# Performance work log

Measured on AMD Instinct MI355X. Metric: run time of the kernel, lower is better.

## Reference

```python
import jax, jax.numpy as jnp
import numpy as np

N = 100000      # nodes
E = 1600000     # edges
NG = 512        # graphs in batch
FIN = 7         # in_features
HID = 128       # hidden_channels
OUT = 2         # outfeatures


def setup_inputs() -> dict:
    key = jax.random.key(0)
    ks = jax.random.split(key, 16)
    x = jax.random.normal(ks[0], (N, FIN), jnp.float32)
    edge_index = jax.random.randint(ks[1], (2, E), 0, N, dtype=jnp.int64)
    batch = jnp.sort(jax.random.randint(ks[2], (N,), 0, NG, dtype=jnp.int64))

    def lin_w(k, fan_in, fan_out):
        # glorot-ish init, scale irrelevant for correctness baseline
        return jax.random.normal(k, (fan_in, fan_out), jnp.float32) / np.sqrt(fan_in).astype(np.float32)

    W1 = lin_w(ks[3], FIN, HID); b1 = jnp.zeros((HID,), jnp.float32)
    W2 = lin_w(ks[4], HID, HID); b2 = jnp.zeros((HID,), jnp.float32)
    W3 = lin_w(ks[5], HID, HID); b3 = jnp.zeros((HID,), jnp.float32)
    W4 = lin_w(ks[6], HID, HID); b4 = jnp.zeros((HID,), jnp.float32)
    Wlin = lin_w(ks[7], HID, OUT); blin = jnp.zeros((OUT,), jnp.float32)
    return dict(x=x, edge_index=edge_index, batch=batch,
                W1=W1, b1=b1, W2=W2, b2=b2, W3=W3, b3=b3, W4=W4, b4=b4,
                Wlin=Wlin, blin=blin)


def gcn_conv(h, W, b, src, dst, n):
    # PyG GCNConv: h' = D^{-1/2} (A + I) D^{-1/2} (h W) + b
    # src/dst already include self-loops
    h = h @ W
    deg = jax.ops.segment_sum(jnp.ones(src.shape[0], h.dtype), dst, num_segments=n)
    dinv = jnp.where(deg > 0, jax.lax.rsqrt(deg), jnp.zeros_like(deg))
    norm = dinv[src] * dinv[dst]                       # [E+N]
    agg = jax.ops.segment_sum(norm[:, None] * h[src], dst, num_segments=n)
    return agg + b


def reference(x, edge_index, batch, W1, b1, W2, b2, W3, b3, W4, b4, Wlin, blin):
    loop = jnp.arange(N, dtype=edge_index.dtype)
    src = jnp.concatenate([edge_index[0], loop])       # add self-loops
    dst = jnp.concatenate([edge_index[1], loop])

    h = gcn_conv(x, W1, b1, src, dst, N)
    for W, b in ((W2, b2), (W3, b3), (W4, b4)):
        h = jax.nn.relu(h)
        h = gcn_conv(h, W, b, src, dst, N)

    # global mean pool per graph
    sums = jax.ops.segment_sum(h, batch, num_segments=NG)
    cnt = jax.ops.segment_sum(jnp.ones((N,), h.dtype), batch, num_segments=NG)
    pooled = sums / jnp.maximum(cnt, 1.0)[:, None]     # [NG, HID]

    # dropout is identity in eval mode
    return pooled @ Wlin + blin                        # [NG, OUT]
```

## Files before the change

### kernel.cpp

```cpp
#include <hip/hip_runtime.h>
#include <hip/hip_bf16.h>

#define N_NODES 100000
#define E_EDGES 1600000
#define NG 512
#define FIN 7
#define HID 128
#define NBUCK 782
#define NBLK_SC 256
#define CHUNK 6250
#define TLEN (NBUCK * NBLK_SC)
#define NCH 196
#define MMX_GRID 782
#define AGGW_GRID 25000

typedef __attribute__((ext_vector_type(8))) short bf16x8;
typedef __attribute__((ext_vector_type(4))) float f32x4;

__device__ __forceinline__ float bf_lo(unsigned int u) { return __uint_as_float(u << 16); }
__device__ __forceinline__ float bf_hi(unsigned int u) { return __uint_as_float(u & 0xffff0000u); }
__device__ __forceinline__ unsigned int f2bf_rne(float f) {
    unsigned int x = __float_as_uint(f);
    return (x + 0x7fffu + ((x >> 16) & 1u)) >> 16;
}
__device__ __forceinline__ unsigned int pack_bf2(float lo, float hi) {
    return f2bf_rne(lo) | (f2bf_rne(hi) << 16);
}


__global__ __launch_bounds__(256) void k_hist2(const int* __restrict__ eidx,
                                               int* __restrict__ table,
                                               const float* __restrict__ W4,
                                               const float* __restrict__ b4,
                                               const float* __restrict__ Wlin,
                                               const float* __restrict__ blin,
                                               float* __restrict__ Wc,
                                               float* __restrict__ bc,
                                               float* __restrict__ pooled,
                                               const float* __restrict__ W2,
                                               const float* __restrict__ W3,
                                               unsigned short* __restrict__ WT2,
                                               unsigned short* __restrict__ WT3) {
    __shared__ int h[NBUCK];
    int blk = blockIdx.x, t = threadIdx.x;
    if (blk >= NBLK_SC) {
        int r = blk - NBLK_SC;
        if (r < 64) {
            float4 z = {0.f, 0.f, 0.f, 0.f};
            *(float4*)&pooled[(r * 256 + t) * 4] = z;
        } else if (r == 64) {
            int k = t >> 1, o = t & 1;
            float acc = 0.f;
            for (int j = 0; j < HID; ++j) acc += W4[k * HID + j] * Wlin[j * 2 + o];
            Wc[k * 2 + o] = acc;
            if (k == 0) {
                float b = blin[o];
                for (int j = 0; j < HID; ++j) b += b4[j] * Wlin[j * 2 + o];
                bc[o] = b;
            }
        } else if (r < 129) {
            int idx = (r - 65) * 256 + t;
            int k = idx >> 7, n = idx & 127;
            WT2[n * 128 + k] = (unsigned short)f2bf_rne(W2[idx]);
        } else {
            int idx = (r - 129) * 256 + t;
            int k = idx >> 7, n = idx & 127;
            WT3[n * 128 + k] = (unsigned short)f2bf_rne(W3[idx]);
        }
        return;
    }
    for (int i = t; i < NBUCK; i += 256) h[i] = 0;
    __syncthreads();
    int e0 = blk * CHUNK, e1 = e0 + CHUNK;
    for (int e = e0 + t; e < e1; e += 256)
        atomicAdd(&h[eidx[E_EDGES + e] >> 7], 1);
    __syncthreads();
    for (int i = t; i < NBUCK; i += 256)
        table[i * NBLK_SC + blk] = h[i];
}

__global__ void k_blocksum(const int* __restrict__ table, int* __restrict__ partial) {
    __shared__ int s[256];
    int b = blockIdx.x, t = threadIdx.x;
    int base = b * 1024;
    int sum = 0;
    for (int i = t; i < 1024; i += 256) {
        int idx = base + i;
        sum += (idx < TLEN) ? table[idx] : 0;
    }
    s[t] = sum; __syncthreads();
    for (int st = 128; st > 0; st >>= 1) {
        if (t < st) s[t] += s[t + st];
        __syncthreads();
    }
    if (t == 0) partial[b] = s[0];
}

__global__ void k_scan_blk(int* __restrict__ partial, int* __restrict__ bucketBase,
                           int* __restrict__ rowptr) {
    __shared__ int s[256];
    int t = threadIdx.x;
    int v = (t < NCH) ? partial[t] : 0;
    s[t] = v; __syncthreads();
    for (int st = 1; st < 256; st <<= 1) {
        int a = (t >= st) ? s[t - st] : 0;
        __syncthreads();
        s[t] += a;
        __syncthreads();
    }
    if (t < NCH) partial[t] = s[t] - v;
    if (t == 0) { bucketBase[NBUCK] = E_EDGES; rowptr[N_NODES] = E_EDGES; }
}

__global__ void k_scan_final(int* __restrict__ table, const int* __restrict__ partial,
                             int* __restrict__ bucketBase) {
    __shared__ int s[1024];
    int b = blockIdx.x, t = threadIdx.x;
    int idx = b * 1024 + t;
    int v = (idx < TLEN) ? table[idx] : 0;
    s[t] = v; __syncthreads();
    for (int st = 1; st < 1024; st <<= 1) {
        int add = (t >= st) ? s[t - st] : 0;
        __syncthreads();
        s[t] += add;
        __syncthreads();
    }
    if (idx < TLEN) {
        int ex = partial[b] + s[t] - v;
        table[idx] = ex;
        if ((idx & (NBLK_SC - 1)) == 0) bucketBase[idx / NBLK_SC] = ex;
    }
}

__global__ __launch_bounds__(256) void k_scatter2(const int* __restrict__ eidx,
                                                  const int* __restrict__ table,
                                                  unsigned int* __restrict__ ebuf) {
    __shared__ int loff[NBUCK];
    int blk = blockIdx.x, t = threadIdx.x;
    for (int i = t; i < NBUCK; i += 256) loff[i] = table[i * NBLK_SC + blk];
    __syncthreads();
    int e0 = blk * CHUNK, e1 = e0 + CHUNK;
    for (int e = e0 + t; e < e1; e += 256) {
        int s = eidx[e];
        int d = eidx[E_EDGES + e];
        int p = atomicAdd(&loff[d >> 7], 1);
        ebuf[p] = ((unsigned int)(d & 127) << 17) | (unsigned int)s;
    }
}

__global__ __launch_bounds__(256) void k_bucket(const unsigned int* __restrict__ ebuf,
                                                const int* __restrict__ bucketBase,
                                                int* __restrict__ rowptr,
                                                float* __restrict__ dinv,
                                                int* __restrict__ col) {
    __shared__ int scnt[128], soff[128], scur[128];
    int b = blockIdx.x, t = threadIdx.x;
    int bbase = bucketBase[b], bend = bucketBase[b + 1];
    if (t < 128) { scnt[t] = 0; scur[t] = 0; }
    __syncthreads();
    for (int e = bbase + t; e < bend; e += 256) {
        unsigned int rec = ebuf[e];
        atomicAdd(&scnt[rec >> 17], 1);
    }
    __syncthreads();
    if (t < 128) soff[t] = scnt[t];
    __syncthreads();
    for (int st = 1; st < 128; st <<= 1) {
        int a = (t < 128 && t >= st) ? soff[t - st] : 0;
        __syncthreads();
        if (t < 128) soff[t] += a;
        __syncthreads();
    }
    if (t < 128) {
        int ex = soff[t] - scnt[t];
        int node = b * 128 + t;
        if (node < N_NODES) {
            rowptr[node] = bbase + ex;
            dinv[node] = rsqrtf((float)(scnt[t] + 1));
        }
        soff[t] = ex;
    }
    __syncthreads();
    for (int e = bbase + t; e < bend; e += 256) {
        unsigned int rec = ebuf[e];
        int dl = rec >> 17;
        int s = rec & 0x1FFFF;
        int p = bbase + soff[dl] + atomicAdd(&scur[dl], 1);
        col[p] = s;
    }
}


__global__ __launch_bounds__(256) void k_l1(const float* __restrict__ x,
                                            const float* __restrict__ W1,
                                            const float* __restrict__ b1,
                                            const int* __restrict__ rowptr,
                                            const int* __restrict__ col,
                                            const float* __restrict__ dinv,
                                            unsigned int* __restrict__ g1) {
    __shared__ float axs[32][8];
    __shared__ float w1s[FIN * HID];
    __shared__ float b1s[HID];
    int t = threadIdx.x;
    for (int i = t; i < FIN * HID; i += 256) w1s[i] = W1[i];
    if (t < HID) b1s[t] = b1[t];

    int lane = t & 63, wave = t >> 6;
    int sub = lane >> 3, f = lane & 7;
    int node = blockIdx.x * 32 + wave * 8 + sub;
    bool valid = node < N_NODES;
    float di = valid ? dinv[node] : 0.f;
    float a = (valid && f < 7) ? di * x[node * FIN + f] : 0.f;
    int e0 = valid ? rowptr[node] : 0;
    int e1 = valid ? rowptr[node + 1] : 0;
    for (int base = e0; base < e1; base += 8) {
        int mm = e1 - base; if (mm > 8) mm = 8;
        int sc = (f < mm) ? col[base + f] : 0;
        for (int j = 0; j < mm; ++j) {
            int s = __shfl(sc, sub * 8 + j);
            float v = (f < 7) ? x[s * FIN + f] : dinv[s];
            float ds = __shfl(v, sub * 8 + 7);
            if (f < 7) a += ds * v;
        }
    }
    axs[wave * 8 + sub][f] = (f < 7) ? di * a : 0.f;
    __syncthreads();

    int nl = t >> 3, fb = t & 7;
    int gnode = blockIdx.x * 32 + nl;
    if (gnode < N_NODES) {
        float av[FIN];
        #pragma unroll
        for (int k = 0; k < FIN; ++k) av[k] = axs[nl][k];
        float dsc = dinv[gnode];
        unsigned int outp[8];
        #pragma unroll
        for (int p = 0; p < 8; ++p) {
            int fo = fb * 16 + p * 2;
            float acc0 = b1s[fo], acc1 = b1s[fo + 1];
            #pragma unroll
            for (int k = 0; k < FIN; ++k) {
                acc0 += av[k] * w1s[k * HID + fo];
                acc1 += av[k] * w1s[k * HID + fo + 1];
            }
            outp[p] = pack_bf2(dsc * fmaxf(acc0, 0.f), dsc * fmaxf(acc1, 0.f));
        }
        *(uint4*)&g1[(size_t)gnode * 64 + fb * 8] = *(uint4*)&outp[0];
        *(uint4*)&g1[(size_t)gnode * 64 + fb * 8 + 4] = *(uint4*)&outp[4];
    }
}


__global__ __launch_bounds__(256) void k_aggW(const unsigned int* __restrict__ gIn,
                                              unsigned int* __restrict__ gOut,
                                              const int* __restrict__ rowptr,
                                              const int* __restrict__ colv,
                                              const float* __restrict__ dinv) {
    int wid = (blockIdx.x * blockDim.x + threadIdx.x) >> 6;
    int lane = threadIdx.x & 63;
    if (wid >= N_NODES) return;
    int i = wid;
    float di = dinv[i];
    int e0 = rowptr[i], e1 = rowptr[i + 1];
    int cv = colv[e0 + lane];
    unsigned int v = gIn[(size_t)i * 64 + lane];
    float ax = bf_lo(v), ay = bf_hi(v);

    for (int base = e0; base < e1; base += 64) {
        int m = e1 - base; if (m > 64) m = 64;
        int cvn = cv;
        if (base + 64 < e1) cvn = colv[base + 64 + lane];
        int j = 0;
        for (; j + 7 < m; j += 8) {
            int s0 = __shfl(cv, j),     s1 = __shfl(cv, j + 1);
            int s2 = __shfl(cv, j + 2), s3 = __shfl(cv, j + 3);
            int s4 = __shfl(cv, j + 4), s5 = __shfl(cv, j + 5);
            int s6 = __shfl(cv, j + 6), s7 = __shfl(cv, j + 7);
            unsigned int u0 = gIn[(size_t)s0 * 64 + lane];
            unsigned int u1 = gIn[(size_t)s1 * 64 + lane];
            unsigned int u2 = gIn[(size_t)s2 * 64 + lane];
            unsigned int u3 = gIn[(size_t)s3 * 64 + lane];
            unsigned int u4 = gIn[(size_t)s4 * 64 + lane];
            unsigned int u5 = gIn[(size_t)s5 * 64 + lane];
            unsigned int u6 = gIn[(size_t)s6 * 64 + lane];
            unsigned int u7 = gIn[(size_t)s7 * 64 + lane];
            ax += bf_lo(u0); ay += bf_hi(u0);
            ax += bf_lo(u1); ay += bf_hi(u1);
            ax += bf_lo(u2); ay += bf_hi(u2);
            ax += bf_lo(u3); ay += bf_hi(u3);
            ax += bf_lo(u4); ay += bf_hi(u4);
            ax += bf_lo(u5); ay += bf_hi(u5);
            ax += bf_lo(u6); ay += bf_hi(u6);
            ax += bf_lo(u7); ay += bf_hi(u7);
        }
        for (; j + 3 < m; j += 4) {
            int s0 = __shfl(cv, j),     s1 = __shfl(cv, j + 1);
            int s2 = __shfl(cv, j + 2), s3 = __shfl(cv, j + 3);
            unsigned int u0 = gIn[(size_t)s0 * 64 + lane];
            unsigned int u1 = gIn[(size_t)s1 * 64 + lane];
            unsigned int u2 = gIn[(size_t)s2 * 64 + lane];
            unsigned int u3 = gIn[(size_t)s3 * 64 + lane];
            ax += bf_lo(u0); ay += bf_hi(u0);
            ax += bf_lo(u1); ay += bf_hi(u1);
            ax += bf_lo(u2); ay += bf_hi(u2);
            ax += bf_lo(u3); ay += bf_hi(u3);
        }
        for (; j < m; ++j) {
            int s0 = __shfl(cv, j);
            unsigned int u0 = gIn[(size_t)s0 * 64 + lane];
            ax += bf_lo(u0); ay += bf_hi(u0);
        }
        cv = cvn;
    }
    gOut[(size_t)i * 64 + lane] = pack_bf2(di * ax, di * ay);
}


__global__ __launch_bounds__(256) void k_mmx(const unsigned int* __restrict__ gIn,
                                             const unsigned short* __restrict__ WTg,
                                             const float* __restrict__ bias,
                                             const float* __restrict__ dinv,
                                             unsigned int* __restrict__ outg) {
    __shared__ unsigned short sbuf[128 * 136];
    int t = threadIdx.x;
    for (int i = t * 8; i < 128 * 128; i += 256 * 8) {
        int n = i >> 7, k = i & 127;
        uint4 val = *(const uint4*)(WTg + i);
        *(uint4*)(sbuf + n * 136 + k) = val;
    }

    int lane = t & 63, wave = t >> 6;
    int m = lane & 15, quad = lane >> 4;
    int nodeBase = blockIdx.x * 128 + wave * 32;
    const short* gs = (const short*)gIn;

    float bi[8];
    #pragma unroll
    for (int nt = 0; nt < 8; ++nt) bi[nt] = bias[nt * 16 + m];

    f32x4 acc[2][8];
    #pragma unroll
    for (int gi = 0; gi < 2; ++gi)
        #pragma unroll
        for (int nt = 0; nt < 8; ++nt)
            acc[gi][nt] = (f32x4){0.f, 0.f, 0.f, 0.f};

    __syncthreads();

    #pragma unroll
    for (int kc = 0; kc < 4; ++kc) {
        bf16x8 ah[2];
        #pragma unroll
        for (int gi = 0; gi < 2; ++gi) {
            int node = nodeBase + gi * 16 + m;
            bf16x8 h = {0, 0, 0, 0, 0, 0, 0, 0};
            if (node < N_NODES)
                h = *(const bf16x8*)(gs + (size_t)node * 128 + kc * 32 + quad * 8);
            ah[gi] = h;
        }
        #pragma unroll
        for (int nt = 0; nt < 8; ++nt) {
            bf16x8 b = *(const bf16x8*)(sbuf + (nt * 16 + m) * 136 + kc * 32 + quad * 8);
            #pragma unroll
            for (int gi = 0; gi < 2; ++gi)
                acc[gi][nt] = __builtin_amdgcn_mfma_f32_16x16x32_bf16(ah[gi], b, acc[gi][nt], 0, 0, 0);
        }
    }

    __syncthreads();
    #pragma unroll
    for (int gi = 0; gi < 2; ++gi)
        #pragma unroll
        for (int r = 0; r < 4; ++r) {
            int nl = wave * 32 + gi * 16 + quad * 4 + r;
            int node = blockIdx.x * 128 + nl;
            float di = (node < N_NODES) ? dinv[node] : 0.f;
            #pragma unroll
            for (int nt = 0; nt < 8; ++nt) {
                float vv = acc[gi][nt][r] + bi[nt];
                sbuf[nl * 132 + nt * 16 + m] = (unsigned short)f2bf_rne(di * fmaxf(vv, 0.f));
            }
        }
    __syncthreads();
    for (int i = t; i < 128 * 32; i += 256) {
        int nl = i >> 5, p = i & 31;
        int node = blockIdx.x * 128 + nl;
        if (node < N_NODES) {
            uint2 val = *(const uint2*)(sbuf + nl * 132 + p * 4);
            *(uint2*)&outg[(size_t)node * 64 + p * 2] = val;
        }
    }
}


__global__ __launch_bounds__(256) void k_poolsum(const unsigned int* __restrict__ aggB,
                                                 const int* __restrict__ batch,
                                                 float* __restrict__ pooled) {
    int wid = (blockIdx.x * blockDim.x + threadIdx.x) >> 6;
    int lane = threadIdx.x & 63;
    int n0 = wid * 16;
    if (n0 >= N_NODES) return;
    int n1 = n0 + 16; if (n1 > N_NODES) n1 = N_NODES;
    int curg = batch[n0];
    float ax = 0.f, ay = 0.f;
    for (int n = n0; n < n1; ++n) {
        int g = batch[n];
        if (g != curg) {
            atomicAdd(&pooled[curg * HID + 2 * lane], ax);
            atomicAdd(&pooled[curg * HID + 2 * lane + 1], ay);
            ax = 0.f; ay = 0.f; curg = g;
        }
        unsigned int u = aggB[(size_t)n * 64 + lane];
        ax += bf_lo(u); ay += bf_hi(u);
    }
    atomicAdd(&pooled[curg * HID + 2 * lane], ax);
    atomicAdd(&pooled[curg * HID + 2 * lane + 1], ay);
}


__global__ void k_head(const float* __restrict__ pooled, const int* __restrict__ batch,
                       const float* __restrict__ Wc, const float* __restrict__ bc,
                       const float* __restrict__ blin, float* __restrict__ out) {
    int wid = (blockIdx.x * blockDim.x + threadIdx.x) >> 6;
    int lane = threadIdx.x & 63;
    if (wid >= NG) return;
    int g = wid;
    int lo = 0, hi = N_NODES;
    while (lo < hi) { int mid = (lo + hi) >> 1; if (batch[mid] < g) lo = mid + 1; else hi = mid; }
    int start = lo;
    hi = N_NODES;
    while (lo < hi) { int mid = (lo + hi) >> 1; if (batch[mid] < g + 1) lo = mid + 1; else hi = mid; }
    int cnt = lo - start;
    float invc = (cnt > 0) ? 1.0f / (float)cnt : 0.f;
    float px = pooled[g * HID + 2 * lane] * invc;
    float py = pooled[g * HID + 2 * lane + 1] * invc;

    #pragma unroll
    for (int o = 0; o < 2; ++o) {
        float v = px * Wc[(2 * lane) * 2 + o] + py * Wc[(2 * lane + 1) * 2 + o];
        #pragma unroll
        for (int s = 32; s > 0; s >>= 1) v += __shfl_down(v, s);
        if (lane == 0) out[g * 2 + o] = (cnt > 0) ? (v + bc[o]) : blin[o];
    }
}


extern "C" void kernel_launch(void* const* d_in, const int* in_sizes, int n_in,
                              void* d_out, int out_size, void* d_ws, size_t ws_size,
                              hipStream_t stream) {
    const float* x    = (const float*)d_in[0];
    const int*   eidx = (const int*)d_in[1];
    const int*   batch= (const int*)d_in[2];
    const float* W1   = (const float*)d_in[3];
    const float* b1   = (const float*)d_in[4];
    const float* W2   = (const float*)d_in[5];
    const float* b2   = (const float*)d_in[6];
    const float* W3   = (const float*)d_in[7];
    const float* b3   = (const float*)d_in[8];
    const float* W4   = (const float*)d_in[9];
    const float* b4   = (const float*)d_in[10];
    const float* Wlin = (const float*)d_in[11];
    const float* blin = (const float*)d_in[12];
    float* out = (float*)d_out;

    char* ws = (char*)d_ws;
    size_t off = 0;
    auto carve = [&](size_t bytes) { char* p = ws + off; off = (off + bytes + 255) & ~(size_t)255; return p; };
    int*   rowptr    = (int*)carve((size_t)(N_NODES + 1) * 4);
    float* dinv      = (float*)carve((size_t)N_NODES * 4);
    int*   col       = (int*)carve((size_t)E_EDGES * 4);
    unsigned int* ebuf = (unsigned int*)carve((size_t)E_EDGES * 4);
    int*   table     = (int*)carve((size_t)TLEN * 4);
    int*   partial   = (int*)carve((size_t)NCH * 4);
    int*   bucketBase= (int*)carve((size_t)(NBUCK + 1) * 4);
    unsigned int* gA = (unsigned int*)carve((size_t)N_NODES * 64 * 4);
    unsigned int* gB = (unsigned int*)carve((size_t)N_NODES * 64 * 4);
    float* pooled    = (float*)carve((size_t)NG * HID * 4);
    float* Wc        = (float*)carve((size_t)HID * 2 * 4);
    float* bc        = (float*)carve(2 * 4);
    unsigned short* WT2 = (unsigned short*)carve((size_t)HID * HID * 2);
    unsigned short* WT3 = (unsigned short*)carve((size_t)HID * HID * 2);
    (void)ws_size; (void)n_in; (void)in_sizes; (void)out_size;

    const int BLK = 256;
    int gridL1 = (N_NODES + 31) / 32;
    int gridPS = ((N_NODES + 15) / 16 * 64 + BLK - 1) / BLK;
    int gridHead = (NG * 64 + BLK - 1) / BLK;

    k_hist2<<<NBLK_SC + 193, BLK, 0, stream>>>(eidx, table, W4, b4, Wlin, blin,
                                               Wc, bc, pooled, W2, W3, WT2, WT3);
    k_blocksum<<<NCH, BLK, 0, stream>>>(table, partial);
    k_scan_blk<<<1, 256, 0, stream>>>(partial, bucketBase, rowptr);
    k_scan_final<<<NCH, 1024, 0, stream>>>(table, partial, bucketBase);
    k_scatter2<<<NBLK_SC, BLK, 0, stream>>>(eidx, table, ebuf);
    k_bucket<<<NBUCK, BLK, 0, stream>>>(ebuf, bucketBase, rowptr, dinv, col);

    k_l1<<<gridL1, BLK, 0, stream>>>(x, W1, b1, rowptr, col, dinv, gA);

    k_aggW<<<AGGW_GRID, BLK, 0, stream>>>(gA, gB, rowptr, col, dinv);
    k_mmx<<<MMX_GRID, BLK, 0, stream>>>(gB, WT2, b2, dinv, gA);
    k_aggW<<<AGGW_GRID, BLK, 0, stream>>>(gA, gB, rowptr, col, dinv);
    k_mmx<<<MMX_GRID, BLK, 0, stream>>>(gB, WT3, b3, dinv, gA);
    k_aggW<<<AGGW_GRID, BLK, 0, stream>>>(gA, gB, rowptr, col, dinv);

    k_poolsum<<<gridPS, BLK, 0, stream>>>(gB, batch, pooled);
    k_head<<<gridHead, BLK, 0, stream>>>(pooled, batch, Wc, bc, blin, out);
}
```

Before: 407.8 us.

## Prescale x by dinv into padded layout and use wave-per-node layer-1 gather

k_bucket now writes a padded 8-float copy of x already multiplied by dinv, so layer 1 no longer has to load dinv[s] for each neighbour. k_l1 is rewritten to give each node one wavefront: eight groups of eight lanes gather eight neighbours at a time with aligned 32-byte row reads, combine the partial sums with xor shuffles, then apply W1 per lane without shared-memory staging. This is meant to cut scattered loads and improve memory parallelism, at the cost of an extra 3.2MB buffer and more blocks. The grid is hard-coded to 25000 blocks of 4 nodes, which exactly covers N, and no bounds check remains.

```diff
diff --git a/kernel.cpp b/kernel.cpp
--- a/kernel.cpp
+++ b/kernel.cpp
@@ -13,6 +13,7 @@
 #define NCH 196
 #define MMX_GRID 782
 #define AGGW_GRID 25000
+#define L1_GRID 25000
 
 typedef __attribute__((ext_vector_type(8))) short bf16x8;
 typedef __attribute__((ext_vector_type(4))) float f32x4;
@@ -152,7 +153,9 @@
                                                 const int* __restrict__ bucketBase,
                                                 int* __restrict__ rowptr,
                                                 float* __restrict__ dinv,
-                                                int* __restrict__ col) {
+                                                int* __restrict__ col,
+                                                const float* __restrict__ x,
+                                                float* __restrict__ xs) {
     __shared__ int scnt[128], soff[128], scur[128];
     int b = blockIdx.x, t = threadIdx.x;
     int bbase = bucketBase[b], bend = bucketBase[b + 1];
@@ -171,12 +174,14 @@
         if (t < 128) soff[t] += a;
         __syncthreads();
     }
+    float dval = 0.f;
     if (t < 128) {
         int ex = soff[t] - scnt[t];
         int node = b * 128 + t;
         if (node < N_NODES) {
             rowptr[node] = bbase + ex;
-            dinv[node] = rsqrtf((float)(scnt[t] + 1));
+            dval = rsqrtf((float)(scnt[t] + 1));
+            dinv[node] = dval;
         }
         soff[t] = ex;
     }
@@ -188,66 +193,79 @@
         int p = bbase + soff[dl] + atomicAdd(&scur[dl], 1);
         col[p] = s;
     }
-}
-
-
-__global__ __launch_bounds__(256) void k_l1(const float* __restrict__ x,
+    if (t < 128) {
+        int node = b * 128 + t;
+        if (node < N_NODES) {
+            float4 v0, v1;
+            v0.x = dval * x[node * 7 + 0];
+            v0.y = dval * x[node * 7 + 1];
+            v0.z = dval * x[node * 7 + 2];
+            v0.w = dval * x[node * 7 + 3];
+            v1.x = dval * x[node * 7 + 4];
+            v1.y = dval * x[node * 7 + 5];
+            v1.z = dval * x[node * 7 + 6];
+            v1.w = 0.f;
+            *(float4*)&xs[node * 8] = v0;
+            *(float4*)&xs[node * 8 + 4] = v1;
+        }
+    }
+}
+
+
+__global__ __launch_bounds__(256) void k_l1(const float* __restrict__ xs,
                                             const float* __restrict__ W1,
                                             const float* __restrict__ b1,
                                             const int* __restrict__ rowptr,
                                             const int* __restrict__ col,
                                             const float* __restrict__ dinv,
                                             unsigned int* __restrict__ g1) {
-    __shared__ float axs[32][8];
     __shared__ float w1s[FIN * HID];
     __shared__ float b1s[HID];
     int t = threadIdx.x;
     for (int i = t; i < FIN * HID; i += 256) w1s[i] = W1[i];
     if (t < HID) b1s[t] = b1[t];
+    __syncthreads();
 
     int lane = t & 63, wave = t >> 6;
-    int sub = lane >> 3, f = lane & 7;
-    int node = blockIdx.x * 32 + wave * 8 + sub;
-    bool valid = node < N_NODES;
-    float di = valid ? dinv[node] : 0.f;
-    float a = (valid && f < 7) ? di * x[node * FIN + f] : 0.f;
-    int e0 = valid ? rowptr[node] : 0;
-    int e1 = valid ? rowptr[node + 1] : 0;
-    for (int base = e0; base < e1; base += 8) {
-        int mm = e1 - base; if (mm > 8) mm = 8;
-        int sc = (f < mm) ? col[base + f] : 0;
-        for (int j = 0; j < mm; ++j) {
-            int s = __shfl(sc, sub * 8 + j);
-            float v = (f < 7) ? x[s * FIN + f] : dinv[s];
-            float ds = __shfl(v, sub * 8 + 7);
-            if (f < 7) a += ds * v;
-        }
-    }
-    axs[wave * 8 + sub][f] = (f < 7) ? di * a : 0.f;
-    __syncthreads();
-
-    int nl = t >> 3, fb = t & 7;
-    int gnode = blockIdx.x * 32 + nl;
-    if (gnode < N_NODES) {
-        float av[FIN];
-        #pragma unroll
-        for (int k = 0; k < FIN; ++k) av[k] = axs[nl][k];
-        float dsc = dinv[gnode];
-        unsigned int outp[8];
-        #pragma unroll
-        for (int p = 0; p < 8; ++p) {
-            int fo = fb * 16 + p * 2;
-            float acc0 = b1s[fo], acc1 = b1s[fo + 1];
-            #pragma unroll
-            for (int k = 0; k < FIN; ++k) {
-                acc0 += av[k] * w1s[k * HID + fo];
-                acc1 += av[k] * w1s[k * HID + fo + 1];
-            }
-            outp[p] = pack_bf2(dsc * fmaxf(acc0, 0.f), dsc * fmaxf(acc1, 0.f));
-        }
-        *(uint4*)&g1[(size_t)gnode * 64 + fb * 8] = *(uint4*)&outp[0];
-        *(uint4*)&g1[(size_t)gnode * 64 + fb * 8 + 4] = *(uint4*)&outp[4];
-    }
+    int g = lane >> 3, r = lane & 7;
+    int node = blockIdx.x * 4 + wave;
+    float di = dinv[node];
+    float acc = (g == 0) ? xs[node * 8 + r] : 0.f;
+    int e0 = rowptr[node], e1 = rowptr[node + 1];
+
+    for (int base = e0; base < e1; base += 64) {
+        int m = e1 - base; if (m > 64) m = 64;
+        int cv = col[base + lane];
+        int j = 0;
+        for (; j + 8 <= m; j += 8) {
+            int s = __shfl(cv, j + g);
+            acc += xs[s * 8 + r];
+        }
+        if (j < m) {
+            int jg = j + g;
+            int idx = (jg < m) ? jg : j;
+            int s = __shfl(cv, idx);
+            float u = xs[s * 8 + r];
+            if (jg < m) acc += u;
+        }
+    }
+    acc += __shfl_xor(acc, 8);
+    acc += __shfl_xor(acc, 16);
+    acc += __shfl_xor(acc, 32);
+    acc *= di;
+
+    float av[FIN];
+    #pragma unroll
+    for (int k = 0; k < FIN; ++k) av[k] = __shfl(acc, k);
+    float2 bb = *(const float2*)&b1s[2 * lane];
+    float acc0 = bb.x, acc1 = bb.y;
+    #pragma unroll
+    for (int k = 0; k < FIN; ++k) {
+        float2 w = *(const float2*)&w1s[k * HID + 2 * lane];
+        acc0 += av[k] * w.x;
+        acc1 += av[k] * w.y;
+    }
+    g1[(size_t)node * 64 + lane] = pack_bf2(di * fmaxf(acc0, 0.f), di * fmaxf(acc1, 0.f));
 }
 
 
@@ -473,6 +491,7 @@
     int*   table     = (int*)carve((size_t)TLEN * 4);
     int*   partial   = (int*)carve((size_t)NCH * 4);
     int*   bucketBase= (int*)carve((size_t)(NBUCK + 1) * 4);
+    float* xs        = (float*)carve((size_t)N_NODES * 8 * 4);
     unsigned int* gA = (unsigned int*)carve((size_t)N_NODES * 64 * 4);
     unsigned int* gB = (unsigned int*)carve((size_t)N_NODES * 64 * 4);
     float* pooled    = (float*)carve((size_t)NG * HID * 4);
@@ -483,7 +502,6 @@
     (void)ws_size; (void)n_in; (void)in_sizes; (void)out_size;
 
     const int BLK = 256;
-    int gridL1 = (N_NODES + 31) / 32;
     int gridPS = ((N_NODES + 15) / 16 * 64 + BLK - 1) / BLK;
     int gridHead = (NG * 64 + BLK - 1) / BLK;
 
@@ -493,9 +511,9 @@
     k_scan_blk<<<1, 256, 0, stream>>>(partial, bucketBase, rowptr);
     k_scan_final<<<NCH, 1024, 0, stream>>>(table, partial, bucketBase);
     k_scatter2<<<NBLK_SC, BLK, 0, stream>>>(eidx, table, ebuf);
-    k_bucket<<<NBUCK, BLK, 0, stream>>>(ebuf, bucketBase, rowptr, dinv, col);
-
-    k_l1<<<gridL1, BLK, 0, stream>>>(x, W1, b1, rowptr, col, dinv, gA);
+    k_bucket<<<NBUCK, BLK, 0, stream>>>(ebuf, bucketBase, rowptr, dinv, col, x, xs);
+
+    k_l1<<<L1_GRID, BLK, 0, stream>>>(xs, W1, b1, rowptr, col, dinv, gA);
 
     k_aggW<<<AGGW_GRID, BLK, 0, stream>>>(gA, gB, rowptr, col, dinv);
     k_mmx<<<MMX_GRID, BLK, 0, stream>>>(gB, WT2, b2, dinv, gA);
```

After: 422.6 us. 3.6% more time.
